# Kernel tuning notes

Hardware: AMD Instinct MI355X
Metric: run time of the kernel (lower is better)

The kernel has to match this reference:

```python
import jax, jax.numpy as jnp
import numpy as np

B, IN, H = 8192, 512, 512


def _binarize(w):
    # sign() forward with straight-through gradient (ebnn Binarize)
    return w + jax.lax.stop_gradient(jnp.sign(w) - w)


def setup_inputs() -> dict:
    key = jax.random.key(0)
    ks = jax.random.split(key, 7)
    stdv = 1.0 / np.sqrt(H)
    return {
        "x": jax.random.normal(ks[0], (B, IN), jnp.float32),
        "hx": jax.random.normal(ks[1], (B, H), jnp.float32),
        "cx": jax.random.normal(ks[2], (B, H), jnp.float32),
        "W_ih": jax.random.uniform(ks[3], (4 * H, IN), jnp.float32, -stdv, stdv),
        "W_hh": jax.random.uniform(ks[4], (4 * H, H), jnp.float32, -stdv, stdv),
        "bias_ih": jax.random.uniform(ks[5], (4 * H,), jnp.float32, -stdv, stdv),
        "bias_hh": jax.random.uniform(ks[6], (4 * H,), jnp.float32, -stdv, stdv),
    }


def reference(x, hx, cx, W_ih, W_hh, bias_ih, bias_hh):
    # gates: [B, 4H] = x @ sign(W_ih)^T + b_ih + hx @ sign(W_hh)^T + b_hh
    gates = (jnp.einsum("bi,gi->bg", x, _binarize(W_ih)) + bias_ih
             + jnp.einsum("bh,gh->bg", hx, _binarize(W_hh)) + bias_hh)
    ingate, forgetgate, cellgate, outgate = jnp.split(gates, 4, axis=1)
    cy = jax.nn.sigmoid(forgetgate) * cx + jax.nn.sigmoid(ingate) * jnp.tanh(cellgate)
    hy = jax.nn.sigmoid(outgate) * jnp.tanh(cy)
    return (hy, cy)
```

## Files before the change

### kernel.cpp

```cpp
#include <hip/hip_runtime.h>
#include <hip/hip_bf16.h>
#include <stdint.h>


typedef __attribute__((ext_vector_type(4))) int int4x;
typedef __attribute__((ext_vector_type(4))) float float4x;

#define B_DIM 8192
#define H_DIM 512

__device__ __forceinline__ float bf2f(uint16_t u) {
  return __uint_as_float(((uint32_t)u) << 16);
}
__device__ __forceinline__ uint16_t f2bf(float f) {
  uint32_t u = __float_as_uint(f);
  return (uint16_t)((u + 0x7FFFu + ((u >> 16) & 1u)) >> 16);
}
__device__ __forceinline__ float sigm(float x) { return 1.0f / (1.0f + __expf(-x)); }
__device__ __forceinline__ float tanh_f(float x) { return 2.0f / (1.0f + __expf(-2.0f * x)) - 1.0f; }

__device__ __forceinline__ int detect_f32(const void* x) {
  const int l = threadIdx.x & 63;
  uint32_t wrd = ((const uint32_t*)x)[l];
  uint32_t e0 = (wrd >> 7) & 0xFFu, e1 = (wrd >> 23) & 0xFFu;
  return __ballot(e0 > 0x85u || e1 > 0x85u) != 0ull;
}

__device__ __forceinline__ void quant4(const float* v, uint32_t* hi4, uint32_t* lo4) {
  uint32_t h = 0, lo = 0;
#pragma unroll
  for (int j = 0; j < 4; ++j) {
    float c = fminf(fmaxf(v[j], -8.0f), 8.0f);
    int xf = __float2int_rn(c * 4096.0f);
    xf = xf > 32639 ? 32639 : xf;
    xf = xf < -32768 ? -32768 : xf;
    const int lb = (xf << 24) >> 24;
    const int hb = (xf - lb) >> 8;
    lo |= ((uint32_t)lb & 0xFFu) << (8 * j);
    h |= ((uint32_t)hb & 0xFFu) << (8 * j);
  }
  *hi4 = h;
  *lo4 = lo;
}

__global__ __launch_bounds__(256) void prep_kernel(
    const void* __restrict__ x, const void* __restrict__ hx,
    const void* __restrict__ w_ih, const void* __restrict__ w_hh,
    int8_t* __restrict__ Xhi, int8_t* __restrict__ Xlo, int8_t* __restrict__ Bp) {
  __shared__ alignas(16) char lsc[33280];
  const int isF32 = detect_f32(x);
  const int t = threadIdx.x;
  const int w = t >> 6, l = t & 63;
  const int isX = blockIdx.x < 512;
  const int grp = isX ? blockIdx.x : (blockIdx.x - 512);

#pragma unroll
  for (int rr = 0; rr < 4; ++rr) {
    const int r = w * 4 + rr;
    long rowbase;
    if (isX) rowbase = (long)(grp * 16 + r) * 512;
    else     rowbase = (long)((grp & 3) * 512 + (grp >> 2) * 16 + r) * 512;
#pragma unroll
    for (int src = 0; src < 2; ++src) {
      const void* sp_ = isX ? (src ? hx : x) : (src ? w_hh : w_ih);
#pragma unroll
      for (int q = 0; q < 2; ++q) {
        const int k = src * 512 + q * 256 + l * 4;
        float v[4];
        if (isF32) {
          float4x f = *(const float4x*)((const float*)sp_ + rowbase + q * 256 + l * 4);
          v[0] = f[0]; v[1] = f[1]; v[2] = f[2]; v[3] = f[3];
        } else {
          const uint16_t* s = (const uint16_t*)sp_ + rowbase + q * 256 + l * 4;
#pragma unroll
          for (int j = 0; j < 4; ++j) v[j] = bf2f(s[j]);
        }
        if (isX) {
          uint32_t h4, lo4;
          quant4(v, &h4, &lo4);
          *(uint32_t*)(lsc + r * 1040 + k) = h4;
          *(uint32_t*)(lsc + 16640 + r * 1040 + k) = lo4;
        } else {
          uint32_t s4 = 0;
#pragma unroll
          for (int j = 0; j < 4; ++j) {
            const int sv = v[j] > 0.f ? 1 : (v[j] < 0.f ? -1 : 0);
            s4 |= ((uint32_t)sv & 0xFFu) << (8 * j);
          }
          *(uint32_t*)(lsc + r * 1040 + k) = s4;
        }
      }
    }
  }
  __syncthreads();
  const int kt = t >> 4, quad = (t >> 2) & 3, rb = (t & 3) * 4;
  const int loff = kt * 64 + quad * 16;
  if (isX) {
    int4x h[4], lo[4];
#pragma unroll
    for (int i = 0; i < 4; ++i) {
      h[i] = *(const int4x*)(lsc + (rb + i) * 1040 + loff);
      lo[i] = *(const int4x*)(lsc + 16640 + (rb + i) * 1040 + loff);
    }
    int4x* dh = (int4x*)(Xhi + (long)grp * 16384 + t * 64);
    int4x* dl = (int4x*)(Xlo + (long)grp * 16384 + t * 64);
#pragma unroll
    for (int i = 0; i < 4; ++i) { dh[i] = h[i]; dl[i] = lo[i]; }
  } else {
    int4x s[4];
#pragma unroll
    for (int i = 0; i < 4; ++i)
      s[i] = *(const int4x*)(lsc + (rb + i) * 1040 + loff);
    int4x* db = (int4x*)(Bp + (long)grp * 16384 + t * 64);
#pragma unroll
    for (int i = 0; i < 4; ++i) db[i] = s[i];
  }
}

__global__ __launch_bounds__(512) void blstm_gemm_kernel(
    const int8_t* __restrict__ Xhi, const int8_t* __restrict__ Xlo,
    const int8_t* __restrict__ Bp, const void* __restrict__ b_ih,
    const void* __restrict__ b_hh, const void* __restrict__ cx,
    const void* __restrict__ xdet, void* __restrict__ out) {
  __shared__ alignas(16) char lds[24576];
  const int tid = threadIdx.x;
  const int l = tid & 63, w = tid >> 6;
  const int lrow = l & 15, lq = l >> 4;
  const int wy = w >> 1, wx = w & 1;
  const int isF32 = detect_f32(xdet);
  const int bid = blockIdx.x;
  const int by = (bid & 7) * 8 + ((bid >> 3) & 7);
  const int bx = bid >> 6;

  const int8_t* sp[3];
  int dof[3];
#pragma unroll
  for (int i = 0; i < 3; ++i) {
    const int c = w * 3 + i;
    if (c < 8) {
      sp[i] = Xhi + ((long)(by * 8 + c) * 16) * 1024 + l * 16;
      dof[i] = c * 1024 + l * 16;
    } else if (c < 16) {
      sp[i] = Xlo + ((long)(by * 8 + (c - 8)) * 16) * 1024 + l * 16;
      dof[i] = 8192 + (c - 8) * 1024 + l * 16;
    } else {
      sp[i] = Bp + ((long)(bx * 8 + (c - 16)) * 16) * 1024 + l * 16;
      dof[i] = 16384 + (c - 16) * 1024 + l * 16;
    }
  }

  int4x acch[2][4], accl[2][4];
#pragma unroll
  for (int mt = 0; mt < 2; ++mt)
#pragma unroll
    for (int g = 0; g < 4; ++g) {
      acch[mt][g] = (int4x){0, 0, 0, 0};
      accl[mt][g] = (int4x){0, 0, 0, 0};
    }

  int4x pre[3];
#pragma unroll
  for (int i = 0; i < 3; ++i) {
    pre[i] = *(const int4x*)sp[i];
    sp[i] += 1024;
  }

  for (int ks = 0; ks < 16; ++ks) {
    __syncthreads();
#pragma unroll
    for (int i = 0; i < 3; ++i)
      *(int4x*)(lds + dof[i]) = pre[i];
    if (ks < 15) {
#pragma unroll
      for (int i = 0; i < 3; ++i) {
        pre[i] = *(const int4x*)sp[i];
        sp[i] += 1024;
      }
    }
    __syncthreads();
    int4x ah[2], al[2], b[4];
#pragma unroll
    for (int mt = 0; mt < 2; ++mt) {
      ah[mt] = *(const int4x*)(lds + (wy * 2 + mt) * 1024 + l * 16);
      al[mt] = *(const int4x*)(lds + 8192 + (wy * 2 + mt) * 1024 + l * 16);
    }
#pragma unroll
    for (int g = 0; g < 4; ++g)
      b[g] = *(const int4x*)(lds + 16384 + (wx * 4 + g) * 1024 + l * 16);
#pragma unroll
    for (int mt = 0; mt < 2; ++mt)
#pragma unroll
      for (int g = 0; g < 4; ++g) {
        acch[mt][g] = __builtin_amdgcn_mfma_i32_16x16x64_i8(ah[mt], b[g], acch[mt][g], 0, 0, 0);
        accl[mt][g] = __builtin_amdgcn_mfma_i32_16x16x64_i8(al[mt], b[g], accl[mt][g], 0, 0, 0);
      }
  }

  const long CYo = (long)B_DIM * H_DIM;
  const int c = bx * 32 + wx * 16 + lrow;
  float biasv[4];
#pragma unroll
  for (int g = 0; g < 4; ++g) {
    if (isF32)
      biasv[g] = ((const float*)b_ih)[g * 512 + c] + ((const float*)b_hh)[g * 512 + c];
    else
      biasv[g] = bf2f(((const uint16_t*)b_ih)[g * 512 + c]) + bf2f(((const uint16_t*)b_hh)[g * 512 + c]);
  }
  float* outF = (float*)out;
  uint16_t* outB = (uint16_t*)out;
#pragma unroll
  for (int mt = 0; mt < 2; ++mt) {
#pragma unroll
    for (int r = 0; r < 4; ++r) {
      const int row = by * 128 + wy * 32 + mt * 16 + lq * 4 + r;
      const long cidx = (long)row * H_DIM + c;
      float vg[4];
#pragma unroll
      for (int g = 0; g < 4; ++g)
        vg[g] = fmaf((float)acch[mt][g][r], 0.0625f,
                     fmaf((float)accl[mt][g][r], 2.44140625e-4f, biasv[g]));
      const float cxv = isF32 ? ((const float*)cx)[cidx] : bf2f(((const uint16_t*)cx)[cidx]);
      const float ig = sigm(vg[0]), fg = sigm(vg[1]), og = sigm(vg[3]);
      const float cg = tanh_f(vg[2]);
      const float cy = fg * cxv + ig * cg;
      const float hy = og * tanh_f(cy);
      if (isF32) {
        outF[cidx] = hy;
        outF[CYo + cidx] = cy;
      } else {
        outB[cidx] = f2bf(hy);
        outB[CYo + cidx] = f2bf(cy);
      }
    }
  }
}

extern "C" void kernel_launch(void* const* d_in, const int* in_sizes, int n_in,
                              void* d_out, int out_size, void* d_ws, size_t ws_size,
                              hipStream_t stream) {
  const void* x = d_in[0];
  const void* hx = d_in[1];
  const void* cx = d_in[2];
  const void* W_ih = d_in[3];
  const void* W_hh = d_in[4];
  const void* b_ih = d_in[5];
  const void* b_hh = d_in[6];
  char* ws = (char*)d_ws;
  int8_t* Xhi = (int8_t*)ws;
  int8_t* Xlo = (int8_t*)(ws + 8388608);
  int8_t* Bp = (int8_t*)(ws + 16777216);

  prep_kernel<<<640, 256, 0, stream>>>(x, hx, W_ih, W_hh, Xhi, Xlo, Bp);
  blstm_gemm_kernel<<<1024, 512, 0, stream>>>(Xhi, Xlo, Bp, b_ih, b_hh, cx, x, d_out);
}
```

Before: 158.5 us.

## Load A fragments directly to registers and double-buffer B in LDS

The GEMM kernel moves to 256-thread blocks with 64-row tiles, so the grid doubles to 2048 blocks. Each wave now loads its A (hi/lo) MFMA fragments straight from global memory into registers. Only the shared B tile is staged through a double-buffered LDS region, with one barrier per k-step instead of two. This aims to cut LDS traffic and barrier stalls and to raise occupancy, at the cost of more redundant global reads of B across blocks and more register pressure.

```diff
diff --git a/kernel.cpp b/kernel.cpp
--- a/kernel.cpp
+++ b/kernel.cpp
@@ -117,36 +117,35 @@
   }
 }
 
-__global__ __launch_bounds__(512) void blstm_gemm_kernel(
+__global__ __launch_bounds__(256, 3) void blstm_gemm_kernel(
     const int8_t* __restrict__ Xhi, const int8_t* __restrict__ Xlo,
     const int8_t* __restrict__ Bp, const void* __restrict__ b_ih,
     const void* __restrict__ b_hh, const void* __restrict__ cx,
     const void* __restrict__ xdet, void* __restrict__ out) {
-  __shared__ alignas(16) char lds[24576];
+  __shared__ alignas(16) char lds[16384];
   const int tid = threadIdx.x;
   const int l = tid & 63, w = tid >> 6;
   const int lrow = l & 15, lq = l >> 4;
   const int wy = w >> 1, wx = w & 1;
   const int isF32 = detect_f32(xdet);
   const int bid = blockIdx.x;
-  const int by = (bid & 7) * 8 + ((bid >> 3) & 7);
-  const int bx = bid >> 6;
-
-  const int8_t* sp[3];
-  int dof[3];
-#pragma unroll
-  for (int i = 0; i < 3; ++i) {
-    const int c = w * 3 + i;
-    if (c < 8) {
-      sp[i] = Xhi + ((long)(by * 8 + c) * 16) * 1024 + l * 16;
-      dof[i] = c * 1024 + l * 16;
-    } else if (c < 16) {
-      sp[i] = Xlo + ((long)(by * 8 + (c - 8)) * 16) * 1024 + l * 16;
-      dof[i] = 8192 + (c - 8) * 1024 + l * 16;
-    } else {
-      sp[i] = Bp + ((long)(bx * 8 + (c - 16)) * 16) * 1024 + l * 16;
-      dof[i] = 16384 + (c - 16) * 1024 + l * 16;
-    }
+  const int by = (bid & 7) * 16 + ((bid >> 3) & 15);
+  const int bx = bid >> 7;
+
+  const int8_t* ap[4];
+#pragma unroll
+  for (int mt = 0; mt < 2; ++mt) {
+    const long t16 = ((long)(by * 4 + wy * 2 + mt) << 14) + l * 16;
+    ap[mt] = Xhi + t16;
+    ap[2 + mt] = Xlo + t16;
+  }
+  const int8_t* bp[2];
+  int dof[2];
+#pragma unroll
+  for (int i = 0; i < 2; ++i) {
+    const int c = w * 2 + i;
+    bp[i] = Bp + ((long)(bx * 8 + c) << 14) + l * 16;
+    dof[i] = c * 1024 + l * 16;
   }
 
   int4x acch[2][4], accl[2][4];
@@ -158,42 +157,41 @@
       accl[mt][g] = (int4x){0, 0, 0, 0};
     }
 
-  int4x pre[3];
-#pragma unroll
-  for (int i = 0; i < 3; ++i) {
-    pre[i] = *(const int4x*)sp[i];
-    sp[i] += 1024;
-  }
-
+  int4x bst[2][2];
+  int4x afr[2][4];
+#pragma unroll
+  for (int i = 0; i < 2; ++i) { bst[0][i] = *(const int4x*)bp[i]; bp[i] += 1024; }
+#pragma unroll
+  for (int i = 0; i < 4; ++i) { afr[0][i] = *(const int4x*)ap[i]; ap[i] += 1024; }
+#pragma unroll
+  for (int i = 0; i < 2; ++i) *(int4x*)(lds + dof[i]) = bst[0][i];
+  asm volatile("s_waitcnt lgkmcnt(0)\n\ts_barrier" ::: "memory");
+
+#pragma unroll
   for (int ks = 0; ks < 16; ++ks) {
-    __syncthreads();
-#pragma unroll
-    for (int i = 0; i < 3; ++i)
-      *(int4x*)(lds + dof[i]) = pre[i];
+    const int cur = ks & 1, nxt = cur ^ 1;
     if (ks < 15) {
 #pragma unroll
-      for (int i = 0; i < 3; ++i) {
-        pre[i] = *(const int4x*)sp[i];
-        sp[i] += 1024;
+      for (int i = 0; i < 2; ++i) { bst[nxt][i] = *(const int4x*)bp[i]; bp[i] += 1024; }
+#pragma unroll
+      for (int i = 0; i < 4; ++i) { afr[nxt][i] = *(const int4x*)ap[i]; ap[i] += 1024; }
+    }
+    int4x b[4];
+#pragma unroll
+    for (int g = 0; g < 4; ++g)
+      b[g] = *(const int4x*)(lds + cur * 8192 + (wx * 4 + g) * 1024 + l * 16);
+#pragma unroll
+    for (int mt = 0; mt < 2; ++mt)
+#pragma unroll
+      for (int g = 0; g < 4; ++g) {
+        acch[mt][g] = __builtin_amdgcn_mfma_i32_16x16x64_i8(afr[cur][mt], b[g], acch[mt][g], 0, 0, 0);
+        accl[mt][g] = __builtin_amdgcn_mfma_i32_16x16x64_i8(afr[cur][2 + mt], b[g], accl[mt][g], 0, 0, 0);
       }
-    }
-    __syncthreads();
-    int4x ah[2], al[2], b[4];
-#pragma unroll
-    for (int mt = 0; mt < 2; ++mt) {
-      ah[mt] = *(const int4x*)(lds + (wy * 2 + mt) * 1024 + l * 16);
-      al[mt] = *(const int4x*)(lds + 8192 + (wy * 2 + mt) * 1024 + l * 16);
-    }
-#pragma unroll
-    for (int g = 0; g < 4; ++g)
-      b[g] = *(const int4x*)(lds + 16384 + (wx * 4 + g) * 1024 + l * 16);
-#pragma unroll
-    for (int mt = 0; mt < 2; ++mt)
-#pragma unroll
-      for (int g = 0; g < 4; ++g) {
-        acch[mt][g] = __builtin_amdgcn_mfma_i32_16x16x64_i8(ah[mt], b[g], acch[mt][g], 0, 0, 0);
-        accl[mt][g] = __builtin_amdgcn_mfma_i32_16x16x64_i8(al[mt], b[g], accl[mt][g], 0, 0, 0);
-      }
+    if (ks < 15) {
+#pragma unroll
+      for (int i = 0; i < 2; ++i) *(int4x*)(lds + nxt * 8192 + dof[i]) = bst[nxt][i];
+      asm volatile("s_waitcnt lgkmcnt(0)\n\ts_barrier" ::: "memory");
+    }
   }
 
   const long CYo = (long)B_DIM * H_DIM;
@@ -212,7 +210,7 @@
   for (int mt = 0; mt < 2; ++mt) {
 #pragma unroll
     for (int r = 0; r < 4; ++r) {
-      const int row = by * 128 + wy * 32 + mt * 16 + lq * 4 + r;
+      const int row = by * 64 + wy * 32 + mt * 16 + lq * 4 + r;
       const long cidx = (long)row * H_DIM + c;
       float vg[4];
 #pragma unroll
@@ -251,5 +249,5 @@
   int8_t* Bp = (int8_t*)(ws + 16777216);
 
   prep_kernel<<<640, 256, 0, stream>>>(x, hx, W_ih, W_hh, Xhi, Xlo, Bp);
-  blstm_gemm_kernel<<<1024, 512, 0, stream>>>(Xhi, Xlo, Bp, b_ih, b_hh, cx, x, d_out);
-}
+  blstm_gemm_kernel<<<2048, 256, 0, stream>>>(Xhi, Xlo, Bp, b_ih, b_hh, cx, x, d_out);
+}
```

After: 154.6 us. -2.5%, faster.

## Double-buffer GEMM LDS tiles with direct global-to-LDS async loads

Applied to the files above, without the earlier changes.

Replaces the register-staged prefetch (global load to VGPRs, then ds_write) with global_load_lds direct-to-LDS copies into a double-buffered 48KB LDS region. The loop drops to one barrier per k-step, is fully unrolled, and raises wave priority around the MFMA block. The aim is to cut the VGPR staging traffic and the second barrier so the next tile's load overlaps the current tile's compute. In exchange the larger LDS footprint may lower occupancy, and the barrier and waitcnt placement in hand-written asm must be correct to avoid races.

```diff
diff --git a/kernel.cpp b/kernel.cpp
--- a/kernel.cpp
+++ b/kernel.cpp
@@ -41,6 +41,12 @@
   }
   *hi4 = h;
   *lo4 = lo;
+}
+
+__device__ __forceinline__ void gload16(const void* g, void* l) {
+  __builtin_amdgcn_global_load_lds(
+      (const __attribute__((address_space(1))) unsigned int*)g,
+      (__attribute__((address_space(3))) unsigned int*)l, 16, 0, 0);
 }
 
 __global__ __launch_bounds__(256) void prep_kernel(
@@ -122,7 +128,7 @@
     const int8_t* __restrict__ Bp, const void* __restrict__ b_ih,
     const void* __restrict__ b_hh, const void* __restrict__ cx,
     const void* __restrict__ xdet, void* __restrict__ out) {
-  __shared__ alignas(16) char lds[24576];
+  __shared__ alignas(16) char lds[49152];
   const int tid = threadIdx.x;
   const int l = tid & 63, w = tid >> 6;
   const int lrow = l & 15, lq = l >> 4;
@@ -132,20 +138,20 @@
   const int by = (bid & 7) * 8 + ((bid >> 3) & 7);
   const int bx = bid >> 6;
 
-  const int8_t* sp[3];
-  int dof[3];
+  const int8_t* csrc[3];
+  int cdst[3];
 #pragma unroll
   for (int i = 0; i < 3; ++i) {
     const int c = w * 3 + i;
     if (c < 8) {
-      sp[i] = Xhi + ((long)(by * 8 + c) * 16) * 1024 + l * 16;
-      dof[i] = c * 1024 + l * 16;
+      csrc[i] = Xhi + (((long)(by * 8 + c)) << 14) + l * 16;
+      cdst[i] = c * 1024;
     } else if (c < 16) {
-      sp[i] = Xlo + ((long)(by * 8 + (c - 8)) * 16) * 1024 + l * 16;
-      dof[i] = 8192 + (c - 8) * 1024 + l * 16;
+      csrc[i] = Xlo + (((long)(by * 8 + (c - 8))) << 14) + l * 16;
+      cdst[i] = 8192 + (c - 8) * 1024;
     } else {
-      sp[i] = Bp + ((long)(bx * 8 + (c - 16)) * 16) * 1024 + l * 16;
-      dof[i] = 16384 + (c - 16) * 1024 + l * 16;
+      csrc[i] = Bp + (((long)(bx * 8 + (c - 16))) << 14) + l * 16;
+      cdst[i] = 16384 + (c - 16) * 1024;
     }
   }
 
@@ -158,35 +164,29 @@
       accl[mt][g] = (int4x){0, 0, 0, 0};
     }
 
-  int4x pre[3];
-#pragma unroll
-  for (int i = 0; i < 3; ++i) {
-    pre[i] = *(const int4x*)sp[i];
-    sp[i] += 1024;
-  }
-
+#pragma unroll
+  for (int i = 0; i < 3; ++i) gload16(csrc[i], lds + cdst[i]);
+  asm volatile("s_waitcnt vmcnt(0)\n\ts_barrier" ::: "memory");
+
+#pragma unroll
   for (int ks = 0; ks < 16; ++ks) {
-    __syncthreads();
-#pragma unroll
-    for (int i = 0; i < 3; ++i)
-      *(int4x*)(lds + dof[i]) = pre[i];
+    const int cb = (ks & 1) * 24576;
+    const int nb = cb ^ 24576;
     if (ks < 15) {
 #pragma unroll
-      for (int i = 0; i < 3; ++i) {
-        pre[i] = *(const int4x*)sp[i];
-        sp[i] += 1024;
-      }
-    }
-    __syncthreads();
+      for (int i = 0; i < 3; ++i)
+        gload16(csrc[i] + (long)(ks + 1) * 1024, lds + nb + cdst[i]);
+    }
     int4x ah[2], al[2], b[4];
 #pragma unroll
     for (int mt = 0; mt < 2; ++mt) {
-      ah[mt] = *(const int4x*)(lds + (wy * 2 + mt) * 1024 + l * 16);
-      al[mt] = *(const int4x*)(lds + 8192 + (wy * 2 + mt) * 1024 + l * 16);
+      ah[mt] = *(const int4x*)(lds + cb + (wy * 2 + mt) * 1024 + l * 16);
+      al[mt] = *(const int4x*)(lds + cb + 8192 + (wy * 2 + mt) * 1024 + l * 16);
     }
 #pragma unroll
     for (int g = 0; g < 4; ++g)
-      b[g] = *(const int4x*)(lds + 16384 + (wx * 4 + g) * 1024 + l * 16);
+      b[g] = *(const int4x*)(lds + cb + 16384 + (wx * 4 + g) * 1024 + l * 16);
+    __builtin_amdgcn_s_setprio(1);
 #pragma unroll
     for (int mt = 0; mt < 2; ++mt)
 #pragma unroll
@@ -194,6 +194,9 @@
         acch[mt][g] = __builtin_amdgcn_mfma_i32_16x16x64_i8(ah[mt], b[g], acch[mt][g], 0, 0, 0);
         accl[mt][g] = __builtin_amdgcn_mfma_i32_16x16x64_i8(al[mt], b[g], accl[mt][g], 0, 0, 0);
       }
+    __builtin_amdgcn_s_setprio(0);
+    if (ks < 15)
+      asm volatile("s_waitcnt vmcnt(0)\n\ts_waitcnt lgkmcnt(0)\n\ts_barrier" ::: "memory");
   }
 
   const long CYo = (long)B_DIM * H_DIM;
```

Result: no change. 156.8 us (-1.1%).
